# Kernel tuning notes

Hardware: AMD Instinct MI355X
Metric: run time of the kernel (lower is better)

Reference implementation:

```python
import jax, jax.numpy as jnp
import numpy as np

B, N, C = 4, 1024, 768          # batch, tokens, embed_dim
D, H, HD, FF = 12, 12, 64, 3072  # depth, heads, head_dim, mlp hidden
LN_EPS = 1e-5


def setup_inputs() -> dict:
    key = jax.random.key(0)
    ks = jax.random.split(key, 12)
    w = lambda i, shape: jax.random.normal(ks[i], shape, jnp.float32) * 0.02
    return {
        "x": jax.random.normal(ks[0], (B, N, C), jnp.float32),
        "pos_x": jax.random.normal(ks[1], (B, N, C), jnp.float32),
        # stacked per-layer params (leading dim D)
        "qkv_w": w(2, (D, 3 * C, C)), "qkv_b": w(3, (D, 3 * C)),
        "proj_w": w(4, (D, C, C)),    "proj_b": w(5, (D, C)),
        "fc1_w": w(6, (D, FF, C)),    "fc1_b": w(7, (D, FF)),
        "fc2_w": w(8, (D, C, FF)),    "fc2_b": w(9, (D, C)),
        "ln1_g": jnp.ones((D, C), jnp.float32), "ln1_b": jnp.zeros((D, C), jnp.float32),
        "ln2_g": jnp.ones((D, C), jnp.float32), "ln2_b": jnp.zeros((D, C), jnp.float32),
        "normf_g": jnp.ones((C,), jnp.float32), "normf_b": jnp.zeros((C,), jnp.float32),
    }


def _ln(x, g, b):
    mu = jnp.mean(x, axis=-1, keepdims=True)
    var = jnp.mean((x - mu) ** 2, axis=-1, keepdims=True)
    return (x - mu) * jax.lax.rsqrt(var + LN_EPS) * g + b


def reference(x, pos_x, qkv_w, qkv_b, proj_w, proj_b, fc1_w, fc1_b, fc2_w, fc2_b,
              ln1_g, ln1_b, ln2_g, ln2_b, normf_g, normf_b):
    scale = 1.0 / jnp.sqrt(jnp.float32(HD))
    x = x + pos_x  # pos added once (add_pos_at_every_layer=False)

    def block(xc, p):
        qw, qb, pw, pb, f1w, f1b, f2w, f2b, g1, b1, g2, b2 = p
        h = _ln(xc, g1, b1)
        qkv = jnp.einsum('bnc,oc->bno', h, qw) + qb            # [B,N,3C]
        qkv = qkv.reshape(B, N, 3, H, HD).transpose(2, 0, 3, 1, 4)
        q, k, v = qkv[0], qkv[1], qkv[2]                       # [B,H,N,HD]
        attn = jax.nn.softmax(jnp.einsum('bhnd,bhmd->bhnm', q, k) * scale, axis=-1)
        o = jnp.einsum('bhnm,bhmd->bhnd', attn, v)
        o = o.transpose(0, 2, 1, 3).reshape(B, N, C)
        xc = xc + (jnp.einsum('bnc,oc->bno', o, pw) + pb)      # residual + proj
        h2 = _ln(xc, g2, b2)
        hid = jax.nn.gelu(jnp.einsum('bnc,fc->bnf', h2, f1w) + f1b, approximate=False)
        ffn = jnp.einsum('bnf,of->bno', hid, f2w) + f2b
        xc = xc + ffn
        return xc, None

    xs = (qkv_w, qkv_b, proj_w, proj_b, fc1_w, fc1_b, fc2_w, fc2_b,
          ln1_g, ln1_b, ln2_g, ln2_b)
    x, _ = jax.lax.scan(block, x, xs)
    return _ln(x, normf_g, normf_b)  # postnorm
```

## Files before the change

kernel.cpp:

```cpp
#include <hip/hip_runtime.h>
#include <hip/hip_bf16.h>
#include <math.h>

typedef __bf16 bf16;
typedef __bf16 bf16x8 __attribute__((ext_vector_type(8)));
typedef __bf16 bf16x4 __attribute__((ext_vector_type(4)));
typedef float  f32x4  __attribute__((ext_vector_type(4)));

#define B_  4
#define N_  1024
#define C_  768
#define H_  12
#define HD_ 64
#define FF_ 3072
#define T_  (B_*N_)
#define D_  12

__device__ __forceinline__ void gld_lds16(const void* g, void* l) {
    __builtin_amdgcn_global_load_lds(
        (const __attribute__((address_space(1))) void*)g,
        (__attribute__((address_space(3))) void*)l, 16, 0, 0);
}

template<typename WT, int MODE>
__global__ __launch_bounds__(256) void gemm_bt(
    const bf16* __restrict__ A, const WT* __restrict__ Bt,
    const float* __restrict__ bias, bf16* __restrict__ out,
    float* __restrict__ resid, int M, int N, int Kfull, int Ks)
{
    __shared__ __align__(16) bf16 lA[128*64];
    __shared__ __align__(16) WT   lB[128*64];
    const int tid  = threadIdx.x;
    const int lane = tid & 63, wave = tid >> 6;
    const int lo = lane & 15, hi = lane >> 4;
    const int wm = wave & 1, wn = wave >> 1;

    const int nblk = gridDim.x;
    const int id2  = (blockIdx.x & 7) * (nblk >> 3) + (blockIdx.x >> 3);
    const int gx = M >> 7, gy = N >> 7;
    const int bx  = id2 % gx;
    const int byz = id2 / gx;
    const int by  = byz % gy;
    const int bz  = byz / gy;
    const int row0 = bx * 128, col0 = by * 128;
    const int k0base = bz * Ks;

    f32x4 acc[4][4];
#pragma unroll
    for (int i = 0; i < 4; i++)
#pragma unroll
        for (int j = 0; j < 4; j++) acc[i][j] = (f32x4){0.f, 0.f, 0.f, 0.f};

    for (int k0 = k0base; k0 < k0base + Ks; k0 += 64) {
#pragma unroll
        for (int r = 0; r < 4; ++r) {
            const int cb    = r * 256 + wave * 64;
            const int chunk = cb + lane;
            const int rw = chunk >> 3, kc = chunk & 7;
            const int kcs = kc ^ (rw & 7);
            gld_lds16(A + (size_t)(row0 + rw) * Kfull + k0 + kcs * 8, lA + cb * 8);
        }
        if constexpr (sizeof(WT) == 2) {
#pragma unroll
            for (int r = 0; r < 4; ++r) {
                const int cb    = r * 256 + wave * 64;
                const int chunk = cb + lane;
                const int rw = chunk >> 3, kc = chunk & 7;
                const int kcs = kc ^ (rw & 7);
                gld_lds16(Bt + (size_t)(col0 + rw) * Kfull + k0 + kcs * 8,
                          (bf16*)lB + cb * 8);
            }
        } else {
#pragma unroll
            for (int r = 0; r < 8; ++r) {
                const int cb    = r * 256 + wave * 64;
                const int chunk = cb + lane;
                const int rw = chunk >> 4, kc = chunk & 15;
                const int kcs = kc ^ ((rw & 7) << 1);
                gld_lds16(Bt + (size_t)(col0 + rw) * Kfull + k0 + kcs * 4,
                          (float*)lB + cb * 4);
            }
        }
        __syncthreads();
#pragma unroll 1
        for (int s = 0; s < 2; ++s) {
            bf16x8 af[4], bfr[4];
#pragma unroll
            for (int i = 0; i < 4; i++) {
                const int rowA = wm * 64 + i * 16 + lo;
                const int ca = (s * 4 + hi) ^ (lo & 7);
                af[i] = *(const bf16x8*)(lA + rowA * 64 + ca * 8);
            }
#pragma unroll
            for (int i = 0; i < 4; i++) {
                const int rowB = wn * 64 + i * 16 + lo;
                if constexpr (sizeof(WT) == 2) {
                    const int cb = (s * 4 + hi) ^ (lo & 7);
                    bfr[i] = *(const bf16x8*)((const bf16*)lB + rowB * 64 + cb * 8);
                } else {
                    const float* base = (const float*)lB + rowB * 64;
                    const int c0 = (s * 8 + hi * 2) ^ ((lo & 7) << 1);
                    const f32x4 u0 = *(const f32x4*)(base + c0 * 4);
                    const f32x4 u1 = *(const f32x4*)(base + (c0 + 1) * 4);
                    bf16x8 f;
#pragma unroll
                    for (int e = 0; e < 4; e++) { f[e] = (bf16)u0[e]; f[4+e] = (bf16)u1[e]; }
                    bfr[i] = f;
                }
            }
#pragma unroll
            for (int mi = 0; mi < 4; mi++)
#pragma unroll
                for (int ni = 0; ni < 4; ni++)
                    acc[mi][ni] = __builtin_amdgcn_mfma_f32_16x16x32_bf16(
                        af[mi], bfr[ni], acc[mi][ni], 0, 0, 0);
        }
        __syncthreads();
    }

    const float bscale = (bz == 0) ? 1.0f : 0.0f;
#pragma unroll
    for (int mi = 0; mi < 4; mi++) {
#pragma unroll
        for (int ni = 0; ni < 4; ni++) {
            const int gcol = col0 + wn * 64 + ni * 16 + lo;
            const float bv = bias[gcol] * bscale;
#pragma unroll
            for (int r = 0; r < 4; r++) {
                const int grow = row0 + wm * 64 + mi * 16 + hi * 4 + r;
                float v = acc[mi][ni][r] + bv;
                if (MODE == 1) v = 0.5f * v * (1.0f + erff(v * 0.70710678118f));
                if (MODE == 2) {
                    atomicAdd(&resid[(size_t)grow * N + gcol], v);
                } else {
                    out[(size_t)grow * N + gcol] = (bf16)v;
                }
            }
        }
    }
}

__global__ __launch_bounds__(256) void cvt_k(
    const float* __restrict__ src, bf16* __restrict__ dst)
{
    const int i = (blockIdx.x * 256 + threadIdx.x) * 8;
    const f32x4 a = *(const f32x4*)(src + i);
    const f32x4 b = *(const f32x4*)(src + i + 4);
    bf16x8 o;
#pragma unroll
    for (int e = 0; e < 4; e++) { o[e] = (bf16)a[e]; o[4 + e] = (bf16)b[e]; }
    *(bf16x8*)(dst + i) = o;
}

template<typename OutT>
__global__ __launch_bounds__(256) void ln_k(
    const float* __restrict__ x, const float* __restrict__ g,
    const float* __restrict__ b, OutT* __restrict__ out)
{
    const int wave = threadIdx.x >> 6, lane = threadIdx.x & 63;
    const int t = blockIdx.x * 4 + wave;
    const float* row = x + (size_t)t * C_;
    f32x4 v[3];
    float s = 0.f, ss = 0.f;
#pragma unroll
    for (int j = 0; j < 3; j++) {
        v[j] = *(const f32x4*)(row + (j * 64 + lane) * 4);
#pragma unroll
        for (int e = 0; e < 4; e++) { s += v[j][e]; ss += v[j][e] * v[j][e]; }
    }
#pragma unroll
    for (int off = 32; off > 0; off >>= 1) {
        s  += __shfl_xor(s, off);
        ss += __shfl_xor(ss, off);
    }
    const float mu  = s * (1.f / 768.f);
    const float var = ss * (1.f / 768.f) - mu * mu;
    const float rs  = rsqrtf(var + 1e-5f);
    OutT* orow = out + (size_t)t * C_;
#pragma unroll
    for (int j = 0; j < 3; j++) {
        const f32x4 gv = *(const f32x4*)(g + (j * 64 + lane) * 4);
        const f32x4 bv = *(const f32x4*)(b + (j * 64 + lane) * 4);
#pragma unroll
        for (int e = 0; e < 4; e++)
            orow[(j * 64 + lane) * 4 + e] = (OutT)((v[j][e] - mu) * rs * gv[e] + bv[e]);
    }
}

__global__ __launch_bounds__(256) void addpos_k(
    const float* __restrict__ x, const float* __restrict__ p, float* __restrict__ o)
{
    const int i = (blockIdx.x * 256 + threadIdx.x) * 4;
    const f32x4 xv = *(const f32x4*)(x + i);
    const f32x4 pv = *(const f32x4*)(p + i);
    f32x4 ov;
#pragma unroll
    for (int e = 0; e < 4; e++) ov[e] = xv[e] + pv[e];
    *(f32x4*)(o + i) = ov;
}

#define SKD_ 72
#define SVK_ 136
#define SPK_ 136
__global__ __launch_bounds__(256) void attn_k(
    const bf16* __restrict__ qkv, bf16* __restrict__ out)
{
    const int id2 = (blockIdx.x & 7) * 96 + (blockIdx.x >> 3);
    const int qt = id2 & 15;
    const int bh = id2 >> 4;
    const int b = bh / H_, h = bh % H_;
    const int lane = threadIdx.x & 63, wave = threadIdx.x >> 6;
    const int lo = lane & 15, hi = lane >> 4;

    __shared__ __align__(16) bf16 lK[128 * SKD_];
    __shared__ __align__(16) bf16 lV[64 * SVK_];
    __shared__ __align__(16) bf16 lP[4][16 * SPK_];

    const size_t tokbase = (size_t)b * N_;

    const bf16* qptr = qkv + (tokbase + qt * 64 + wave * 16 + lo) * (3 * C_) + h * HD_;
    bf16x8 qf0 = *(const bf16x8*)(qptr + hi * 8);
    bf16x8 qf1 = *(const bf16x8*)(qptr + 32 + hi * 8);
#pragma unroll
    for (int e = 0; e < 8; e++) {
        qf0[e] = (bf16)((float)qf0[e] * 0.125f);
        qf1[e] = (bf16)((float)qf1[e] * 0.125f);
    }

    float m_r[4], l_r[4];
    f32x4 oacc[4];
#pragma unroll
    for (int r = 0; r < 4; r++) { m_r[r] = -1e30f; l_r[r] = 0.f; }
#pragma unroll
    for (int di = 0; di < 4; di++) oacc[di] = (f32x4){0.f, 0.f, 0.f, 0.f};

    for (int kt = 0; kt < 8; ++kt) {
        const int kb0 = kt * 128;
#pragma unroll
        for (int r = 0; r < 4; ++r) {
            const int chunk = r * 256 + threadIdx.x;
            const int key = chunk >> 3, dc = chunk & 7;
            const bf16* kp = qkv + (tokbase + kb0 + key) * (3 * C_) + C_ + h * HD_ + dc * 8;
            *(bf16x8*)(lK + key * SKD_ + dc * 8) = *(const bf16x8*)kp;
        }
#pragma unroll
        for (int r = 0; r < 4; ++r) {
            const int chunk = r * 256 + threadIdx.x;
            const int d = chunk & 63, kg = chunk >> 6;
            const bf16* vp = qkv + (tokbase + kb0 + kg * 8) * (3 * C_)
                           + 2 * C_ + h * HD_ + d;
            bf16x8 tv;
#pragma unroll
            for (int i = 0; i < 8; i++) tv[i] = vp[(size_t)i * (3 * C_)];
            *(bf16x8*)(lV + d * SVK_ + kg * 8) = tv;
        }
        __syncthreads();

        f32x4 sacc[8];
#pragma unroll
        for (int kb = 0; kb < 8; kb++) {
            const bf16x8 b0 = *(const bf16x8*)(lK + (kb * 16 + lo) * SKD_ + hi * 8);
            const bf16x8 b1 = *(const bf16x8*)(lK + (kb * 16 + lo) * SKD_ + 32 + hi * 8);
            f32x4 a = (f32x4){0.f, 0.f, 0.f, 0.f};
            a = __builtin_amdgcn_mfma_f32_16x16x32_bf16(qf0, b0, a, 0, 0, 0);
            a = __builtin_amdgcn_mfma_f32_16x16x32_bf16(qf1, b1, a, 0, 0, 0);
            sacc[kb] = a;
        }

        float pm[4], mn[4], ts[4];
#pragma unroll
        for (int r = 0; r < 4; r++) {
            float a0 = fmaxf(fmaxf(sacc[0][r], sacc[1][r]),
                             fmaxf(sacc[2][r], sacc[3][r]));
            float a1 = fmaxf(fmaxf(sacc[4][r], sacc[5][r]),
                             fmaxf(sacc[6][r], sacc[7][r]));
            pm[r] = fmaxf(a0, a1);
            ts[r] = 0.f;
        }
        const int okd = (pm[0] <= m_r[0] + 8.f) && (pm[1] <= m_r[1] + 8.f)
                     && (pm[2] <= m_r[2] + 8.f) && (pm[3] <= m_r[3] + 8.f);
        const bool defer = __all(okd);
        if (defer) {
#pragma unroll
            for (int r = 0; r < 4; r++) mn[r] = m_r[r];
        } else {
#pragma unroll
            for (int r = 0; r < 4; r++) {
                float tm = pm[r];
#pragma unroll
                for (int off = 1; off < 16; off <<= 1)
                    tm = fmaxf(tm, __shfl_xor(tm, off));
                mn[r] = fmaxf(m_r[r], tm);
            }
        }
#pragma unroll
        for (int kb = 0; kb < 8; kb++)
#pragma unroll
            for (int r = 0; r < 4; r++) {
                const float p = __expf(sacc[kb][r] - mn[r]);
                lP[wave][(hi * 4 + r) * SPK_ + kb * 16 + lo] = (bf16)p;
                ts[r] += p;
            }
#pragma unroll
        for (int r = 0; r < 4; r++)
#pragma unroll
            for (int off = 1; off < 16; off <<= 1)
                ts[r] += __shfl_xor(ts[r], off);
        if (defer) {
#pragma unroll
            for (int r = 0; r < 4; r++) l_r[r] += ts[r];
        } else {
            float alpha[4];
#pragma unroll
            for (int r = 0; r < 4; r++) {
                alpha[r] = __expf(m_r[r] - mn[r]);
                l_r[r] = l_r[r] * alpha[r] + ts[r];
                m_r[r] = mn[r];
            }
#pragma unroll
            for (int di = 0; di < 4; di++)
#pragma unroll
                for (int r = 0; r < 4; r++) oacc[di][r] *= alpha[r];
        }

        bf16x8 pa[4];
#pragma unroll
        for (int s = 0; s < 4; s++)
            pa[s] = *(const bf16x8*)(&lP[wave][lo * SPK_ + s * 32 + hi * 8]);
#pragma unroll
        for (int di = 0; di < 4; di++) {
#pragma unroll
            for (int s = 0; s < 4; s++) {
                const bf16x8 v = *(const bf16x8*)(lV + (di * 16 + lo) * SVK_ + s * 32 + hi * 8);
                oacc[di] = __builtin_amdgcn_mfma_f32_16x16x32_bf16(pa[s], v, oacc[di], 0, 0, 0);
            }
        }
        __syncthreads();
    }

    float il[4];
#pragma unroll
    for (int r = 0; r < 4; r++) il[r] = 1.0f / l_r[r];
#pragma unroll
    for (int di = 0; di < 4; di++)
#pragma unroll
        for (int r = 0; r < 4; r++) {
            const size_t tok = tokbase + qt * 64 + wave * 16 + hi * 4 + r;
            out[tok * C_ + h * HD_ + di * 16 + lo] = (bf16)(oacc[di][r] * il[r]);
        }
}

extern "C" void kernel_launch(void* const* d_in, const int* in_sizes, int n_in,
                              void* d_out, int out_size, void* d_ws, size_t ws_size,
                              hipStream_t stream)
{
    const float* x      = (const float*)d_in[0];
    const float* pos_x  = (const float*)d_in[1];
    const float* qkv_w  = (const float*)d_in[2];
    const float* qkv_b  = (const float*)d_in[3];
    const float* proj_w = (const float*)d_in[4];
    const float* proj_b = (const float*)d_in[5];
    const float* fc1_w  = (const float*)d_in[6];
    const float* fc1_b  = (const float*)d_in[7];
    const float* fc2_w  = (const float*)d_in[8];
    const float* fc2_b  = (const float*)d_in[9];
    const float* ln1_g  = (const float*)d_in[10];
    const float* ln1_b  = (const float*)d_in[11];
    const float* ln2_g  = (const float*)d_in[12];
    const float* ln2_b  = (const float*)d_in[13];
    const float* nf_g   = (const float*)d_in[14];
    const float* nf_b   = (const float*)d_in[15];

    char* ws = (char*)d_ws;
    float* xres  = (float*)(ws);
    bf16* hbuf   = (bf16*)(ws + 12582912);
    bf16* qkvbuf = (bf16*)(ws + 18874368);
    bf16* attno  = (bf16*)(ws + 37748736);
    bf16* hid    = (bf16*)(ws + 44040192);
    bf16* wq     = (bf16*)(ws + 69206016);
    bf16* wp     = (bf16*)(ws + 111673344);
    bf16* w1     = (bf16*)(ws + 125829120);
    bf16* w2     = (bf16*)(ws + 182452224);
    const bool usebf16 = ws_size >= (size_t)239075328;

    addpos_k<<<T_ * C_ / 4 / 256, 256, 0, stream>>>(x, pos_x, xres);

    if (usebf16) {
        cvt_k<<<D_ * 3 * C_ * C_ / 2048, 256, 0, stream>>>(qkv_w, wq);
        cvt_k<<<D_ * C_ * C_ / 2048, 256, 0, stream>>>(proj_w, wp);
        cvt_k<<<D_ * FF_ * C_ / 2048, 256, 0, stream>>>(fc1_w, w1);
        cvt_k<<<D_ * C_ * FF_ / 2048, 256, 0, stream>>>(fc2_w, w2);
    }

    const int g_qkv  = (T_/128) * ((3*C_)/128);
    const int g_proj = (T_/128) * (C_/128) * 2;
    const int g_fc1  = (T_/128) * (FF_/128);
    const int g_fc2  = (T_/128) * (C_/128) * 2;

    for (int L = 0; L < D_; ++L) {
        ln_k<bf16><<<T_ / 4, 256, 0, stream>>>(xres, ln1_g + L * C_, ln1_b + L * C_, hbuf);
        if (usebf16) {
            gemm_bt<bf16,0><<<g_qkv, 256, 0, stream>>>(
                hbuf, wq + (size_t)L * 3 * C_ * C_, qkv_b + (size_t)L * 3 * C_,
                qkvbuf, nullptr, T_, 3 * C_, C_, C_);
        } else {
            gemm_bt<float,0><<<g_qkv, 256, 0, stream>>>(
                hbuf, qkv_w + (size_t)L * 3 * C_ * C_, qkv_b + (size_t)L * 3 * C_,
                qkvbuf, nullptr, T_, 3 * C_, C_, C_);
        }
        attn_k<<<N_ / 64 * B_ * H_, 256, 0, stream>>>(qkvbuf, attno);
        if (usebf16) {
            gemm_bt<bf16,2><<<g_proj, 256, 0, stream>>>(
                attno, wp + (size_t)L * C_ * C_, proj_b + (size_t)L * C_,
                nullptr, xres, T_, C_, C_, C_ / 2);
        } else {
            gemm_bt<float,2><<<g_proj, 256, 0, stream>>>(
                attno, proj_w + (size_t)L * C_ * C_, proj_b + (size_t)L * C_,
                nullptr, xres, T_, C_, C_, C_ / 2);
        }
        ln_k<bf16><<<T_ / 4, 256, 0, stream>>>(xres, ln2_g + L * C_, ln2_b + L * C_, hbuf);
        if (usebf16) {
            gemm_bt<bf16,1><<<g_fc1, 256, 0, stream>>>(
                hbuf, w1 + (size_t)L * FF_ * C_, fc1_b + (size_t)L * FF_,
                hid, nullptr, T_, FF_, C_, C_);
            gemm_bt<bf16,2><<<g_fc2, 256, 0, stream>>>(
                hid, w2 + (size_t)L * C_ * FF_, fc2_b + (size_t)L * C_,
                nullptr, xres, T_, C_, FF_, FF_ / 2);
        } else {
            gemm_bt<float,1><<<g_fc1, 256, 0, stream>>>(
                hbuf, fc1_w + (size_t)L * FF_ * C_, fc1_b + (size_t)L * FF_,
                hid, nullptr, T_, FF_, C_, C_);
            gemm_bt<float,2><<<g_fc2, 256, 0, stream>>>(
                hid, fc2_w + (size_t)L * C_ * FF_, fc2_b + (size_t)L * C_,
                nullptr, xres, T_, C_, FF_, FF_ / 2);
        }
    }
    ln_k<float><<<T_ / 4, 256, 0, stream>>>(xres, nf_g, nf_b, (float*)d_out);
}
```

Before: 2.557 ms.

## Double-buffer LDS tiles in bf16 GEMM and use polynomial erf for GELU

For bf16-weight GEMMs, the LDS A/B tiles are double-buffered so the next K tile's global-to-LDS loads are issued before computing the current tile, with one barrier per iteration. This aims to overlap memory latency with MFMA work, at the cost of twice the LDS per block, which may lower occupancy. Separately, the GELU epilogue replaces erff with an Abramowitz-Stegun polynomial using a reciprocal and fast exp. That approximation has an error near 1e-7, which is below bf16 output precision.

Result: slower. 2.878 ms (+12.6%).

```diff
diff --git a/kernel.cpp b/kernel.cpp
--- a/kernel.cpp
+++ b/kernel.cpp
@@ -22,14 +22,28 @@
         (__attribute__((address_space(3))) void*)l, 16, 0, 0);
 }
 
+__device__ __forceinline__ float gelu_f(float v) {
+    const float ax = fabsf(v) * 0.70710678118f;
+    const float t  = __frcp_rn(1.0f + 0.3275911f * ax);
+    float p = 1.061405429f;
+    p = p * t - 1.453152027f;
+    p = p * t + 1.421413741f;
+    p = p * t - 0.284496736f;
+    p = p * t + 0.254829592f;
+    const float e = p * t * __expf(-ax * ax);
+    const float erfv = (v >= 0.f) ? (1.0f - e) : (e - 1.0f);
+    return 0.5f * v * (1.0f + erfv);
+}
+
 template<typename WT, int MODE>
 __global__ __launch_bounds__(256) void gemm_bt(
     const bf16* __restrict__ A, const WT* __restrict__ Bt,
     const float* __restrict__ bias, bf16* __restrict__ out,
     float* __restrict__ resid, int M, int N, int Kfull, int Ks)
 {
-    __shared__ __align__(16) bf16 lA[128*64];
-    __shared__ __align__(16) WT   lB[128*64];
+    constexpr int NB = (sizeof(WT) == 2) ? 2 : 1;
+    __shared__ __align__(16) bf16 lA[NB][128*64];
+    __shared__ __align__(16) WT   lB[NB][128*64];
     const int tid  = threadIdx.x;
     const int lane = tid & 63, wave = tid >> 6;
     const int lo = lane & 15, hi = lane >> 4;
@@ -44,6 +58,7 @@
     const int bz  = byz / gy;
     const int row0 = bx * 128, col0 = by * 128;
     const int k0base = bz * Ks;
+    const int nt = Ks >> 6;
 
     f32x4 acc[4][4];
 #pragma unroll
@@ -51,15 +66,18 @@
 #pragma unroll
         for (int j = 0; j < 4; j++) acc[i][j] = (f32x4){0.f, 0.f, 0.f, 0.f};
 
-    for (int k0 = k0base; k0 < k0base + Ks; k0 += 64) {
+    auto stageA = [&](int t, int buf) {
 #pragma unroll
         for (int r = 0; r < 4; ++r) {
             const int cb    = r * 256 + wave * 64;
             const int chunk = cb + lane;
             const int rw = chunk >> 3, kc = chunk & 7;
             const int kcs = kc ^ (rw & 7);
-            gld_lds16(A + (size_t)(row0 + rw) * Kfull + k0 + kcs * 8, lA + cb * 8);
-        }
+            gld_lds16(A + (size_t)(row0 + rw) * Kfull + k0base + t * 64 + kcs * 8,
+                      lA[buf] + cb * 8);
+        }
+    };
+    auto stageB = [&](int t, int buf) {
         if constexpr (sizeof(WT) == 2) {
 #pragma unroll
             for (int r = 0; r < 4; ++r) {
@@ -67,8 +85,8 @@
                 const int chunk = cb + lane;
                 const int rw = chunk >> 3, kc = chunk & 7;
                 const int kcs = kc ^ (rw & 7);
-                gld_lds16(Bt + (size_t)(col0 + rw) * Kfull + k0 + kcs * 8,
-                          (bf16*)lB + cb * 8);
+                gld_lds16(Bt + (size_t)(col0 + rw) * Kfull + k0base + t * 64 + kcs * 8,
+                          (bf16*)lB[buf] + cb * 8);
             }
         } else {
 #pragma unroll
@@ -77,11 +95,12 @@
                 const int chunk = cb + lane;
                 const int rw = chunk >> 4, kc = chunk & 15;
                 const int kcs = kc ^ ((rw & 7) << 1);
-                gld_lds16(Bt + (size_t)(col0 + rw) * Kfull + k0 + kcs * 4,
-                          (float*)lB + cb * 4);
-            }
-        }
-        __syncthreads();
+                gld_lds16(Bt + (size_t)(col0 + rw) * Kfull + k0base + t * 64 + kcs * 4,
+                          (float*)lB[buf] + cb * 4);
+            }
+        }
+    };
+    auto compute = [&](int buf) {
 #pragma unroll 1
         for (int s = 0; s < 2; ++s) {
             bf16x8 af[4], bfr[4];
@@ -89,16 +108,16 @@
             for (int i = 0; i < 4; i++) {
                 const int rowA = wm * 64 + i * 16 + lo;
                 const int ca = (s * 4 + hi) ^ (lo & 7);
-                af[i] = *(const bf16x8*)(lA + rowA * 64 + ca * 8);
+                af[i] = *(const bf16x8*)(lA[buf] + rowA * 64 + ca * 8);
             }
 #pragma unroll
             for (int i = 0; i < 4; i++) {
                 const int rowB = wn * 64 + i * 16 + lo;
                 if constexpr (sizeof(WT) == 2) {
-                    const int cb = (s * 4 + hi) ^ (lo & 7);
-                    bfr[i] = *(const bf16x8*)((const bf16*)lB + rowB * 64 + cb * 8);
+                    const int cc = (s * 4 + hi) ^ (lo & 7);
+                    bfr[i] = *(const bf16x8*)((const bf16*)lB[buf] + rowB * 64 + cc * 8);
                 } else {
-                    const float* base = (const float*)lB + rowB * 64;
+                    const float* base = (const float*)lB[buf] + rowB * 64;
                     const int c0 = (s * 8 + hi * 2) ^ ((lo & 7) << 1);
                     const f32x4 u0 = *(const f32x4*)(base + c0 * 4);
                     const f32x4 u1 = *(const f32x4*)(base + (c0 + 1) * 4);
@@ -115,7 +134,25 @@
                     acc[mi][ni] = __builtin_amdgcn_mfma_f32_16x16x32_bf16(
                         af[mi], bfr[ni], acc[mi][ni], 0, 0, 0);
         }
+    };
+
+    if constexpr (NB == 2) {
+        stageA(0, 0); stageB(0, 0);
         __syncthreads();
+        int cur = 0;
+        for (int t = 0; t < nt; ++t) {
+            if (t + 1 < nt) { stageA(t + 1, cur ^ 1); stageB(t + 1, cur ^ 1); }
+            compute(cur);
+            __syncthreads();
+            cur ^= 1;
+        }
+    } else {
+        for (int t = 0; t < nt; ++t) {
+            stageA(t, 0); stageB(t, 0);
+            __syncthreads();
+            compute(0);
+            __syncthreads();
+        }
     }
 
     const float bscale = (bz == 0) ? 1.0f : 0.0f;
@@ -129,7 +166,7 @@
             for (int r = 0; r < 4; r++) {
                 const int grow = row0 + wm * 64 + mi * 16 + hi * 4 + r;
                 float v = acc[mi][ni][r] + bv;
-                if (MODE == 1) v = 0.5f * v * (1.0f + erff(v * 0.70710678118f));
+                if (MODE == 1) v = gelu_f(v);
                 if (MODE == 2) {
                     atomicAdd(&resid[(size_t)grow * N + gcol], v);
                 } else {
```
